# Optimization experiments

Measured on AMD Instinct MI355X. Metric: run time of the kernel, lower is better.

Reference implementation:

```python
import jax, jax.numpy as jnp
import numpy as np

B, T, D = 2, 2048, 1024
H = 16
DK = D // H


def setup_inputs() -> dict:
    key = jax.random.key(0)
    ks = jax.random.split(key, 5)
    s = 1.0 / np.sqrt(D)
    return {
        "x": jax.random.normal(ks[0], (B, T, D), dtype=jnp.float32),
        "Wq": jax.random.normal(ks[1], (D, D), dtype=jnp.float32) * s,
        "bq": jnp.zeros((D,), dtype=jnp.float32),
        "Wk": jax.random.normal(ks[2], (D, D), dtype=jnp.float32) * s,
        "bk": jnp.zeros((D,), dtype=jnp.float32),
        "Wv": jax.random.normal(ks[3], (D, D), dtype=jnp.float32) * s,
        "bv": jnp.zeros((D,), dtype=jnp.float32),
        "Wo": jax.random.normal(ks[4], (D, D), dtype=jnp.float32) * s,
        "bo": jnp.zeros((D,), dtype=jnp.float32),
    }


def reference(x, Wq, bq, Wk, bk, Wv, bv, Wo, bo):
    # projections (torch Linear: x @ W.T + b; here W is stored as (in, out))
    Q = x @ Wq + bq  # (B,T,D)
    K = x @ Wk + bk
    V = x @ Wv + bv
    # split heads -> (B,H,T,dk)
    Q = Q.reshape(B, T, H, DK).transpose(0, 2, 1, 3)
    K = K.reshape(B, T, H, DK).transpose(0, 2, 1, 3)
    V = V.reshape(B, T, H, DK).transpose(0, 2, 1, 3)
    scale = 1.0 / jnp.sqrt(jnp.asarray(DK, dtype=x.dtype))
    scores = jnp.einsum("bhqd,bhkd->bhqk", Q, K) * scale  # (B,H,T,T)
    causal = jnp.tril(jnp.ones((T, T), dtype=bool))
    scores = jnp.where(causal, scores, -jnp.inf)
    weights = jax.nn.softmax(scores, axis=-1)
    # dropout is identity in eval mode
    context = jnp.einsum("bhqk,bhkd->bhqd", weights, V)
    context = context.transpose(0, 2, 1, 3).reshape(B, T, D)
    return context @ Wo + bo
```

## Files before the change

kernel.cpp:

```cpp
#include <hip/hip_runtime.h>
#include <hip/hip_bf16.h>

constexpr int Bc = 2;
constexpr int Tc = 2048;
constexpr int Mc = Bc * Tc;
constexpr float CfQ = 0.18033688011112042f;

typedef __attribute__((ext_vector_type(8))) __bf16 bf16x8;
typedef __attribute__((ext_vector_type(4))) __bf16 bf16x4;
typedef __attribute__((ext_vector_type(4))) float floatx4;

__device__ __forceinline__ void gl_lds16(const void* g, void* l) {
    __builtin_amdgcn_global_load_lds(
        (const __attribute__((address_space(1))) void*)g,
        (__attribute__((address_space(3))) void*)l, 16, 0, 0);
}

__global__ __launch_bounds__(256) void prep_all(const float* __restrict__ x,
                                                const float* __restrict__ Wq,
                                                const float* __restrict__ Wk,
                                                const float* __restrict__ Wv,
                                                const float* __restrict__ Wo,
                                                __bf16* __restrict__ xb,
                                                __bf16* __restrict__ Wqkv,
                                                __bf16* __restrict__ Wot) {
    const int z = blockIdx.z;
    const int tid = threadIdx.x;
    if (z >= 4) {
        const int lb = blockIdx.y * 16 + blockIdx.x;
        const size_t base = ((size_t)(z - 4) * 256 + lb) * 4096;
#pragma unroll
        for (int it = 0; it < 4; ++it) {
            const size_t i = base + (size_t)(it * 256 + tid) * 4;
            const float4 v = *(const float4*)(x + i);
            bf16x4 r;
            r[0] = (__bf16)v.x; r[1] = (__bf16)v.y;
            r[2] = (__bf16)v.z; r[3] = (__bf16)v.w;
            *(bf16x4*)(xb + i) = r;
        }
        return;
    }
    __shared__ float t[64][65];
    const float* W = (z == 0) ? Wq : (z == 1) ? Wk : (z == 2) ? Wv : Wo;
    __bf16* Wt = (z < 3) ? Wqkv + (size_t)z * 1024 * 1024 : Wot;
    const int k0 = blockIdx.y * 64, n0 = blockIdx.x * 64;
    const int c = tid & 63, r0 = tid >> 6;
#pragma unroll
    for (int i = 0; i < 16; ++i)
        t[r0 + i * 4][c] = W[(size_t)(k0 + r0 + i * 4) * 1024 + n0 + c];
    __syncthreads();
#pragma unroll
    for (int i = 0; i < 16; ++i) {
        const int r = r0 + i * 4;
        Wt[(size_t)(n0 + r) * 1024 + k0 + c] = (__bf16)t[c][r];
    }
}

__global__ __launch_bounds__(512, 2) void gemm_qkv(const __bf16* __restrict__ A,
                                                   const __bf16* __restrict__ Bt,
                                                   const float* __restrict__ b0,
                                                   const float* __restrict__ b1,
                                                   const float* __restrict__ b2,
                                                   __bf16* __restrict__ C,
                                                   __bf16* __restrict__ Vt) {
    constexpr int K = 1024, ldc = 2048;
    __shared__ __bf16 As[2][256 * 64];
    __shared__ __bf16 Bs[2][192 * 64];
    const int tid = threadIdx.x, lane = tid & 63, wave = tid >> 6;
    const int wm = wave >> 2, wn = wave & 3;
    const int n = blockIdx.x;
    const int xc = n & 7, ii = n >> 3;
    const int by = 2 * xc + (ii & 1), bx = ii >> 1;
    const int bm = by * 256, bn = bx * 192;
    const __bf16* Ab = A + (size_t)bm * K;
    const __bf16* Bb = Bt + (size_t)bn * K;
    const int quad = lane >> 4, tm = lane & 15;

    floatx4 acc[8][3] = {};

    auto stage = [&](int k0, int sb) {
#pragma unroll
        for (int j = 0; j < 4; ++j) {
            const int s = j * 512 + tid;
            const int row = s >> 3, lc = (s & 7) ^ (row & 7);
            gl_lds16(Ab + (size_t)row * K + k0 + lc * 8, &As[sb][s * 8]);
        }
#pragma unroll
        for (int j = 0; j < 3; ++j) {
            const int s = j * 512 + tid;
            const int row = s >> 3, lc = (s & 7) ^ (row & 7);
            gl_lds16(Bb + (size_t)row * K + k0 + lc * 8, &Bs[sb][s * 8]);
        }
    };

    stage(0, 0);

    for (int st = 0; st < 16; ++st) {
        const int buf = st & 1;
        if (st + 1 < 16) {
            stage((st + 1) * 64, buf ^ 1);
            asm volatile("s_waitcnt vmcnt(7)" ::: "memory");
        } else {
            asm volatile("s_waitcnt vmcnt(0)" ::: "memory");
        }
        __builtin_amdgcn_sched_barrier(0);
        __builtin_amdgcn_s_barrier();

        const __bf16* as = As[buf];
        const __bf16* bs = Bs[buf];
#pragma unroll
        for (int ks = 0; ks < 2; ++ks) {
            bf16x8 bfp[3], afq[8];
#pragma unroll
            for (int n2 = 0; n2 < 3; ++n2) {
                const int r = wn * 48 + n2 * 16 + tm;
                bfp[n2] = *(const bf16x8*)(
                    bs + r * 64 + (((ks * 4 + quad) ^ (r & 7)) * 8));
            }
#pragma unroll
            for (int m8 = 0; m8 < 8; ++m8) {
                const int r = wm * 128 + m8 * 16 + tm;
                afq[m8] = *(const bf16x8*)(
                    as + r * 64 + (((ks * 4 + quad) ^ (r & 7)) * 8));
            }
            __builtin_amdgcn_s_setprio(1);
#pragma unroll
            for (int m8 = 0; m8 < 8; ++m8)
#pragma unroll
                for (int n2 = 0; n2 < 3; ++n2)
                    acc[m8][n2] = __builtin_amdgcn_mfma_f32_16x16x32_bf16(
                        afq[m8], bfp[n2], acc[m8][n2], 0, 0, 0);
            __builtin_amdgcn_s_setprio(0);
        }
        __builtin_amdgcn_sched_barrier(0);
        __builtin_amdgcn_s_barrier();
    }

#pragma unroll
    for (int ni = 0; ni < 3; ++ni) {
        const int gc = bn + wn * 48 + ni * 16 + tm;
        const float bias = (gc < 1024) ? b0[gc]
                         : (gc < 2048) ? b1[gc - 1024]
                                       : b2[gc - 2048];
        const float scale = (gc < 1024) ? CfQ : 1.0f;
#pragma unroll
        for (int mi = 0; mi < 8; ++mi) {
            const int gr0 = bm + wm * 128 + mi * 16 + quad * 4;
            if (gc >= 2048) {
                bf16x4 pv;
#pragma unroll
                for (int r = 0; r < 4; ++r) pv[r] = (__bf16)(acc[mi][ni][r] + bias);
                const int bb = gr0 >> 11, tloc = gr0 & 2047;
                const int hh = (gc - 2048) >> 6, dd = gc & 63;
                const int tperm = (tloc & ~63) + ((tloc >> 2) & 3) * 16 +
                                  ((tloc >> 4) & 3) * 4;
                *(bf16x4*)(Vt + ((size_t)(bb * 16 + hh) * 64 + dd) * 2048 + tperm) = pv;
            } else {
#pragma unroll
                for (int r = 0; r < 4; ++r)
                    C[(size_t)(gr0 + r) * ldc + gc] =
                        (__bf16)((acc[mi][ni][r] + bias) * scale);
            }
        }
    }
}

__global__ __launch_bounds__(256) void gemm_out(const __bf16* __restrict__ A,
                                                const __bf16* __restrict__ Bt,
                                                const float* __restrict__ b0,
                                                float* __restrict__ C) {
    constexpr int TN = 64, NI = 2, K = 1024, ldc = 1024;
    __shared__ __bf16 As[2][128 * 32];
    __shared__ __bf16 Bs[2][TN * 32];
    const int tid = threadIdx.x, lane = tid & 63, wave = tid >> 6;
    const int wm = wave & 1, wn = wave >> 1;
    const int bm = blockIdx.y * 128, bn = blockIdx.x * TN;
    const __bf16* Ab = A + (size_t)bm * K;
    const __bf16* Bb = Bt + (size_t)bn * K;
    const int quad = lane >> 4, tm = lane & 15;
    const int xsw = (tm >> 1) & 3;

    floatx4 acc[4][NI] = {};

    auto stage = [&](int k0, int sbuf) {
#pragma unroll
        for (int i = 0; i < 2; ++i) {
            const int s = i * 256 + tid;
            const int row = s >> 2;
            const int lc = (s & 3) ^ ((row >> 1) & 3);
            gl_lds16(Ab + (size_t)row * K + k0 + lc * 8, &As[sbuf][s * 8]);
        }
        {
            const int s = tid;
            const int row = s >> 2;
            const int lc = (s & 3) ^ ((row >> 1) & 3);
            gl_lds16(Bb + (size_t)row * K + k0 + lc * 8, &Bs[sbuf][s * 8]);
        }
    };

    const int nstep = K >> 5;
    stage(0, 0);
    stage(32, 1);

    for (int ks = 0; ks < nstep; ++ks) {
        const int buf = ks & 1;
        if (ks + 1 < nstep) {
            asm volatile("s_waitcnt vmcnt(3)" ::: "memory");
        } else {
            asm volatile("s_waitcnt vmcnt(0)" ::: "memory");
        }
        __builtin_amdgcn_sched_barrier(0);
        __builtin_amdgcn_s_barrier();

        bf16x8 af[4], bfv[NI];
#pragma unroll
        for (int mi = 0; mi < 4; ++mi)
            af[mi] = *(const bf16x8*)(&As[buf][(wm * 64 + mi * 16 + tm) * 32 +
                                               ((quad ^ xsw) * 8)]);
#pragma unroll
        for (int ni = 0; ni < NI; ++ni)
            bfv[ni] = *(const bf16x8*)(&Bs[buf][(wn * (TN / 2) + ni * 16 + tm) * 32 +
                                                ((quad ^ xsw) * 8)]);
        __builtin_amdgcn_s_setprio(1);
#pragma unroll
        for (int mi = 0; mi < 4; ++mi)
#pragma unroll
            for (int ni = 0; ni < NI; ++ni)
                acc[mi][ni] = __builtin_amdgcn_mfma_f32_16x16x32_bf16(
                    af[mi], bfv[ni], acc[mi][ni], 0, 0, 0);
        __builtin_amdgcn_s_setprio(0);
        __builtin_amdgcn_sched_barrier(0);
        __builtin_amdgcn_s_barrier();
        if (ks + 2 < nstep) stage((ks + 2) * 32, buf);
    }

#pragma unroll
    for (int ni = 0; ni < NI; ++ni) {
        const int gc = bn + wn * (TN / 2) + ni * 16 + tm;
        const float bias = b0[gc];
#pragma unroll
        for (int mi = 0; mi < 4; ++mi) {
            const int gr0 = bm + wm * 64 + mi * 16 + quad * 4;
#pragma unroll
            for (int r = 0; r < 4; ++r)
                C[(size_t)(gr0 + r) * ldc + gc] = acc[mi][ni][r] + bias;
        }
    }
}

__global__ __launch_bounds__(512, 4) void attn_mfma(const __bf16* __restrict__ QK,
                                                    const __bf16* __restrict__ Vt,
                                                    __bf16* __restrict__ ctx) {
    constexpr float NEG = -1e30f;

    __shared__ __bf16 Ks[2][2][64 * 64];
    __shared__ __bf16 Vts[2][2][64 * 64];

    const int tid = threadIdx.x, lane = tid & 63, w = tid >> 6;
    const int g = w >> 2, wq = w & 3;
    const int c = lane & 15, quad = lane >> 4;
    const int n = blockIdx.x;
    const int bh = (n & 7) * 4 + ((n >> 3) & 3);
    const int ip = n >> 5;
    const int b = bh >> 4, h = bh & 15;

    const __bf16* Qb = QK + (size_t)(b * Tc) * 2048 + h * 64;
    const __bf16* Kb = Qb + 1024;
    const __bf16* Vtb = Vt + (size_t)bh * 64 * 2048;

    const int sw = c & 7;
    int koff0[4], koff1[4];
#pragma unroll
    for (int ni = 0; ni < 4; ++ni) {
        const int krow = ni * 16 + c;
        koff0[ni] = krow * 64 + (quad ^ sw) * 8;
        koff1[ni] = krow * 64 + ((4 + quad) ^ sw) * 8;
    }
    int voff[4][2];
#pragma unroll
    for (int di = 0; di < 4; ++di) {
        const int vrow = di * 16 + c;
#pragma unroll
        for (int pr = 0; pr < 2; ++pr)
            voff[di][pr] = vrow * 64 + ((quad * 2 + pr) ^ sw) * 8;
    }

    const int srow = tid >> 3;
    const int slc = (tid & 7) ^ (srow & 7);
    const __bf16* kgB = Kb + (size_t)srow * 2048 + slc * 8;
    const __bf16* vgB = Vtb + (size_t)srow * 2048 + slc * 8;

#pragma unroll 1
    for (int ph = 0; ph < 2; ++ph) {
        const int qt = ph ? 31 - ip : ip;
        const int nk = qt + 1;
        const int npair = (nk + 1) >> 1;

        const __bf16* qr = Qb + (size_t)(qt * 64 + wq * 16 + c) * 2048;
        const bf16x8 qf0 = *(const bf16x8*)(qr + quad * 8);
        const bf16x8 qf1 = *(const bf16x8*)(qr + 32 + quad * 8);

        floatx4 lacc = {};
        floatx4 oa[4] = {};

        auto stage = [&](int p, int sbuf) {
            const __bf16* kg = kgB + (size_t)(2 * p) * 64 * 2048;
            const __bf16* vg = vgB + 2 * p * 64;
            __bf16* kd = &Ks[sbuf][0][tid * 8];
            __bf16* vd = &Vts[sbuf][0][tid * 8];
            gl_lds16(kg, kd);
            gl_lds16(kg + (size_t)64 * 2048, kd + 4096);
            gl_lds16(vg, vd);
            gl_lds16(vg + 64, vd + 4096);
        };

        stage(0, 0);
        if (npair > 1) stage(1, 1);

        for (int kp = 0; kp < npair; ++kp) {
            const int buf = kp & 1;
            if (kp + 1 < npair) {
                asm volatile("s_waitcnt vmcnt(4)" ::: "memory");
            } else {
                asm volatile("s_waitcnt vmcnt(0)" ::: "memory");
            }
            __builtin_amdgcn_sched_barrier(0);
            __builtin_amdgcn_s_barrier();

            const int kt = 2 * kp + g;
            if (kt < nk) {
                const __bf16* ks = Ks[buf][g];
                const __bf16* vs = Vts[buf][g];

                float sv[4][4];
                __builtin_amdgcn_s_setprio(1);
#pragma unroll
                for (int ni = 0; ni < 4; ++ni) {
                    const bf16x8 kb0 = *(const bf16x8*)(ks + koff0[ni]);
                    const bf16x8 kb1 = *(const bf16x8*)(ks + koff1[ni]);
                    floatx4 a = {};
                    a = __builtin_amdgcn_mfma_f32_16x16x32_bf16(kb0, qf0, a, 0, 0, 0);
                    a = __builtin_amdgcn_mfma_f32_16x16x32_bf16(kb1, qf1, a, 0, 0, 0);
#pragma unroll
                    for (int r = 0; r < 4; ++r) sv[ni][r] = a[r];
                }
                __builtin_amdgcn_s_setprio(0);

                if (kt == qt) {
#pragma unroll
                    for (int ni = 0; ni < 4; ++ni)
#pragma unroll
                        for (int r = 0; r < 4; ++r)
                            if (ni * 16 + quad * 4 + r > wq * 16 + c) sv[ni][r] = NEG;
                }
#pragma unroll
                for (int ni = 0; ni < 4; ++ni) {
#pragma unroll
                    for (int r = 0; r < 4; ++r) sv[ni][r] = __builtin_exp2f(sv[ni][r]);
                    lacc[0] += sv[ni][0];
                    lacc[1] += sv[ni][1];
                    lacc[2] += sv[ni][2];
                    lacc[3] += sv[ni][3];
                }

                bf16x8 pb[2];
#pragma unroll
                for (int pr = 0; pr < 2; ++pr)
#pragma unroll
                    for (int j = 0; j < 4; ++j) {
                        pb[pr][j] = (__bf16)sv[pr * 2][j];
                        pb[pr][4 + j] = (__bf16)sv[pr * 2 + 1][j];
                    }

                __builtin_amdgcn_s_setprio(1);
#pragma unroll
                for (int di = 0; di < 4; ++di) {
#pragma unroll
                    for (int pr = 0; pr < 2; ++pr) {
                        const bf16x8 vf = *(const bf16x8*)(vs + voff[di][pr]);
                        oa[di] = __builtin_amdgcn_mfma_f32_16x16x32_bf16(
                            vf, pb[pr], oa[di], 0, 0, 0);
                    }
                }
                __builtin_amdgcn_s_setprio(0);
            }
            __builtin_amdgcn_sched_barrier(0);
            __builtin_amdgcn_s_barrier();
            if (kp + 2 < npair) stage(kp + 2, buf);
        }

        __syncthreads();
        float lsum = lacc[0] + lacc[1] + lacc[2] + lacc[3];
        float* sc = (float*)&Ks[0][0][0];
        if (g == 1) {
#pragma unroll
            for (int di = 0; di < 4; ++di)
                *(floatx4*)(sc + wq * 1088 + di * 256 + lane * 4) = oa[di];
            sc[wq * 1088 + 1024 + lane] = lsum;
        }
        __syncthreads();
        if (g == 0) {
#pragma unroll
            for (int di = 0; di < 4; ++di)
                oa[di] += *(const floatx4*)(sc + wq * 1088 + di * 256 + lane * 4);
            lsum += sc[wq * 1088 + 1024 + lane];
            lsum += __shfl_xor(lsum, 16);
            lsum += __shfl_xor(lsum, 32);
            const float inv = 1.f / lsum;
            __bf16* cp = ctx + (size_t)(b * Tc + qt * 64 + wq * 16 + c) * 1024 +
                         h * 64 + quad * 4;
#pragma unroll
            for (int di = 0; di < 4; ++di) {
                bf16x4 rv;
#pragma unroll
                for (int r = 0; r < 4; ++r) rv[r] = (__bf16)(oa[di][r] * inv);
                *(bf16x4*)(cp + di * 16) = rv;
            }
        }
        __syncthreads();
    }
}

extern "C" void kernel_launch(void* const* d_in, const int* in_sizes, int n_in,
                              void* d_out, int out_size, void* d_ws, size_t ws_size,
                              hipStream_t stream) {
    const float* x  = (const float*)d_in[0];
    const float* Wq = (const float*)d_in[1];
    const float* bq = (const float*)d_in[2];
    const float* Wk = (const float*)d_in[3];
    const float* bk = (const float*)d_in[4];
    const float* Wv = (const float*)d_in[5];
    const float* bv = (const float*)d_in[6];
    const float* Wo = (const float*)d_in[7];
    const float* bo = (const float*)d_in[8];

    __bf16* xb   = (__bf16*)d_ws;
    __bf16* Wqkv = xb + (size_t)Mc * 1024;
    __bf16* Wot  = Wqkv + (size_t)3072 * 1024;
    __bf16* QKb  = Wot + (size_t)1024 * 1024;
    __bf16* Vtw  = QKb + (size_t)Mc * 2048;
    __bf16* ctxb = xb;

    prep_all<<<dim3(16, 16, 8), 256, 0, stream>>>(x, Wq, Wk, Wv, Wo,
                                                  xb, Wqkv, Wot);

    gemm_qkv<<<dim3(256), 512, 0, stream>>>(xb, Wqkv, bq, bk, bv, QKb, Vtw);

    attn_mfma<<<dim3(512), 512, 0, stream>>>(QKb, Vtw, ctxb);

    gemm_out<<<dim3(16, 32), 256, 0, stream>>>(ctxb, Wot, bo, (float*)d_out);
}
```

Before: 179.9 us.

## Switch attention to 32x32x16 MFMA with 4-way key split and new V layout

Rewrites the attention inner loop to use 32x32x16 bf16 MFMA tiles, with each wave covering 32 queries and 32-key tiles. Work is split into four key groups per query pair, and partial results are reduced through LDS in two rounds. The V-transpose layout written by the QKV GEMM changes to match the new fragment order. P fragments are rearranged with lane shuffles. The aim is fewer MFMA instructions and LDS reads per FLOP, at the cost of a longer cross-group reduction and the shuffle overhead.

```diff
diff --git a/kernel.cpp b/kernel.cpp
--- a/kernel.cpp
+++ b/kernel.cpp
@@ -9,11 +9,19 @@
 typedef __attribute__((ext_vector_type(8))) __bf16 bf16x8;
 typedef __attribute__((ext_vector_type(4))) __bf16 bf16x4;
 typedef __attribute__((ext_vector_type(4))) float floatx4;
+typedef __attribute__((ext_vector_type(16))) float f32x16;
+typedef __attribute__((ext_vector_type(4))) unsigned int uint4v;
 
 __device__ __forceinline__ void gl_lds16(const void* g, void* l) {
     __builtin_amdgcn_global_load_lds(
         (const __attribute__((address_space(1))) void*)g,
         (__attribute__((address_space(3))) void*)l, 16, 0, 0);
+}
+
+__device__ __forceinline__ unsigned int pkbf(float x, float y) {
+    union { __bf16 h[2]; unsigned int u; } z;
+    z.h[0] = (__bf16)x; z.h[1] = (__bf16)y;
+    return z.u;
 }
 
 __global__ __launch_bounds__(256) void prep_all(const float* __restrict__ x,
@@ -152,9 +160,10 @@
                 for (int r = 0; r < 4; ++r) pv[r] = (__bf16)(acc[mi][ni][r] + bias);
                 const int bb = gr0 >> 11, tloc = gr0 & 2047;
                 const int hh = (gc - 2048) >> 6, dd = gc & 63;
-                const int tperm = (tloc & ~63) + ((tloc >> 2) & 3) * 16 +
-                                  ((tloc >> 4) & 3) * 4;
-                *(bf16x4*)(Vt + ((size_t)(bb * 16 + hh) * 64 + dd) * 2048 + tperm) = pv;
+                const int tt = tloc >> 5, t5 = tloc & 31;
+                const int u = dd & 31, half = dd >> 5;
+                *(bf16x4*)(Vt + ((size_t)(bb * 16 + hh) * 64 + tt) * 2048 +
+                           u * 64 + half * 32 + t5) = pv;
             } else {
 #pragma unroll
                 for (int r = 0; r < 4; ++r)
@@ -253,12 +262,12 @@
                                                     __bf16* __restrict__ ctx) {
     constexpr float NEG = -1e30f;
 
-    __shared__ __bf16 Ks[2][2][64 * 64];
-    __shared__ __bf16 Vts[2][2][64 * 64];
+    __shared__ __bf16 Ks[2][4][32 * 64];
+    __shared__ __bf16 Vts[2][4][32 * 64];
 
     const int tid = threadIdx.x, lane = tid & 63, w = tid >> 6;
-    const int g = w >> 2, wq = w & 3;
-    const int c = lane & 15, quad = lane >> 4;
+    const int g = w >> 1, ws = w & 1;
+    const int col = lane & 31, hi = lane >> 5;
     const int n = blockIdx.x;
     const int bh = (n & 7) * 4 + ((n >> 3) & 3);
     const int ip = n >> 5;
@@ -266,60 +275,64 @@
 
     const __bf16* Qb = QK + (size_t)(b * Tc) * 2048 + h * 64;
     const __bf16* Kb = Qb + 1024;
-    const __bf16* Vtb = Vt + (size_t)bh * 64 * 2048;
-
-    const int sw = c & 7;
-    int koff0[4], koff1[4];
-#pragma unroll
-    for (int ni = 0; ni < 4; ++ni) {
-        const int krow = ni * 16 + c;
-        koff0[ni] = krow * 64 + (quad ^ sw) * 8;
-        koff1[ni] = krow * 64 + ((4 + quad) ^ sw) * 8;
-    }
-    int voff[4][2];
-#pragma unroll
-    for (int di = 0; di < 4; ++di) {
-        const int vrow = di * 16 + c;
-#pragma unroll
-        for (int pr = 0; pr < 2; ++pr)
-            voff[di][pr] = vrow * 64 + ((quad * 2 + pr) ^ sw) * 8;
-    }
-
-    const int srow = tid >> 3;
-    const int slc = (tid & 7) ^ (srow & 7);
-    const __bf16* kgB = Kb + (size_t)srow * 2048 + slc * 8;
-    const __bf16* vgB = Vtb + (size_t)srow * 2048 + slc * 8;
+    const __bf16* Vtb = Vt + (size_t)bh * 131072;
+
+    const int sw7 = lane & 7;
+    int koff[4], voff[2][2];
+#pragma unroll
+    for (int k16 = 0; k16 < 4; ++k16)
+        koff[k16] = col * 64 + (((k16 * 2 + hi) ^ sw7) * 8);
+#pragma unroll
+    for (int dt = 0; dt < 2; ++dt)
+#pragma unroll
+        for (int tc = 0; tc < 2; ++tc)
+            voff[dt][tc] = col * 64 + (((dt * 4 + tc * 2 + hi) ^ sw7) * 8);
+
+    const __bf16* kK[2];
+    const __bf16* kV[2];
+#pragma unroll
+    for (int j = 0; j < 2; ++j) {
+        const int kc = j * 512 + tid;
+        const int gj = kc >> 8;
+        const int wv = kc & 255;
+        const int r = wv >> 3, lc = (wv & 7) ^ (r & 7);
+        kK[j] = Kb + (size_t)(gj * 32 + r) * 2048 + lc * 8;
+        kV[j] = Vtb + (size_t)gj * 2048 + r * 64 + lc * 8;
+    }
 
 #pragma unroll 1
     for (int ph = 0; ph < 2; ++ph) {
         const int qt = ph ? 31 - ip : ip;
-        const int nk = qt + 1;
-        const int npair = (nk + 1) >> 1;
-
-        const __bf16* qr = Qb + (size_t)(qt * 64 + wq * 16 + c) * 2048;
-        const bf16x8 qf0 = *(const bf16x8*)(qr + quad * 8);
-        const bf16x8 qf1 = *(const bf16x8*)(qr + 32 + quad * 8);
+        const int nkt = 2 * qt + 2;
+        const int niter = (nkt + 3) >> 2;
+        const int ktmax = 2 * qt + ws;
+
+        const __bf16* qr = Qb + (size_t)(qt * 64 + ws * 32 + col) * 2048;
+        bf16x8 qf[4];
+#pragma unroll
+        for (int k16 = 0; k16 < 4; ++k16)
+            qf[k16] = *(const bf16x8*)(qr + k16 * 16 + hi * 8);
 
         floatx4 lacc = {};
-        floatx4 oa[4] = {};
-
-        auto stage = [&](int p, int sbuf) {
-            const __bf16* kg = kgB + (size_t)(2 * p) * 64 * 2048;
-            const __bf16* vg = vgB + 2 * p * 64;
-            __bf16* kd = &Ks[sbuf][0][tid * 8];
-            __bf16* vd = &Vts[sbuf][0][tid * 8];
-            gl_lds16(kg, kd);
-            gl_lds16(kg + (size_t)64 * 2048, kd + 4096);
-            gl_lds16(vg, vd);
-            gl_lds16(vg + 64, vd + 4096);
+        f32x16 oa0 = {}, oa1 = {};
+
+        auto stage = [&](int p, int sb) {
+            __bf16* kd = &Ks[sb][0][0];
+            __bf16* vd = &Vts[sb][0][0];
+#pragma unroll
+            for (int j = 0; j < 2; ++j) {
+                const int kc = j * 512 + tid;
+                gl_lds16(kK[j] + (size_t)p * 128 * 2048, kd + kc * 8);
+                gl_lds16(kV[j] + (size_t)p * 8192, vd + kc * 8);
+            }
         };
 
         stage(0, 0);
-        if (npair > 1) stage(1, 1);
-
-        for (int kp = 0; kp < npair; ++kp) {
+        if (niter > 1) stage(1, 1);
+
+        for (int kp = 0; kp < niter; ++kp) {
             const int buf = kp & 1;
-            if (kp + 1 < npair) {
+            if (kp + 1 < niter) {
                 asm volatile("s_waitcnt vmcnt(4)" ::: "memory");
             } else {
                 asm volatile("s_waitcnt vmcnt(0)" ::: "memory");
@@ -327,95 +340,144 @@
             __builtin_amdgcn_sched_barrier(0);
             __builtin_amdgcn_s_barrier();
 
-            const int kt = 2 * kp + g;
-            if (kt < nk) {
-                const __bf16* ks = Ks[buf][g];
-                const __bf16* vs = Vts[buf][g];
-
-                float sv[4][4];
+            const int kt = 4 * kp + g;
+            if (kt <= ktmax) {
+                const __bf16* ks = &Ks[buf][g][0];
+                const __bf16* vs = &Vts[buf][g][0];
+
+                f32x16 acc = {};
                 __builtin_amdgcn_s_setprio(1);
 #pragma unroll
-                for (int ni = 0; ni < 4; ++ni) {
-                    const bf16x8 kb0 = *(const bf16x8*)(ks + koff0[ni]);
-                    const bf16x8 kb1 = *(const bf16x8*)(ks + koff1[ni]);
-                    floatx4 a = {};
-                    a = __builtin_amdgcn_mfma_f32_16x16x32_bf16(kb0, qf0, a, 0, 0, 0);
-                    a = __builtin_amdgcn_mfma_f32_16x16x32_bf16(kb1, qf1, a, 0, 0, 0);
-#pragma unroll
-                    for (int r = 0; r < 4; ++r) sv[ni][r] = a[r];
+                for (int k16 = 0; k16 < 4; ++k16) {
+                    const bf16x8 kb = *(const bf16x8*)(ks + koff[k16]);
+                    acc = __builtin_amdgcn_mfma_f32_32x32x16_bf16(
+                        kb, qf[k16], acc, 0, 0, 0);
                 }
                 __builtin_amdgcn_s_setprio(0);
 
-                if (kt == qt) {
-#pragma unroll
-                    for (int ni = 0; ni < 4; ++ni)
-#pragma unroll
-                        for (int r = 0; r < 4; ++r)
-                            if (ni * 16 + quad * 4 + r > wq * 16 + c) sv[ni][r] = NEG;
-                }
-#pragma unroll
-                for (int ni = 0; ni < 4; ++ni) {
-#pragma unroll
-                    for (int r = 0; r < 4; ++r) sv[ni][r] = __builtin_exp2f(sv[ni][r]);
-                    lacc[0] += sv[ni][0];
-                    lacc[1] += sv[ni][1];
-                    lacc[2] += sv[ni][2];
-                    lacc[3] += sv[ni][3];
-                }
-
-                bf16x8 pb[2];
-#pragma unroll
-                for (int pr = 0; pr < 2; ++pr)
-#pragma unroll
-                    for (int j = 0; j < 4; ++j) {
-                        pb[pr][j] = (__bf16)sv[pr * 2][j];
-                        pb[pr][4 + j] = (__bf16)sv[pr * 2 + 1][j];
+                if (kt == ktmax) {
+#pragma unroll
+                    for (int reg = 0; reg < 16; ++reg) {
+                        const int crow = (reg & 3) + 8 * (reg >> 2) + 4 * hi;
+                        if (crow > col) acc[reg] = NEG;
                     }
+                }
+#pragma unroll
+                for (int reg = 0; reg < 16; ++reg) {
+                    const float p = __builtin_exp2f(acc[reg]);
+                    acc[reg] = p;
+                    lacc[reg & 3] += p;
+                }
+
+                bf16x8 pf[2];
+#pragma unroll
+                for (int tc = 0; tc < 2; ++tc) {
+                    const int c16 = tc * 8;
+                    const unsigned int a0 = pkbf(acc[c16 + 0], acc[c16 + 1]);
+                    const unsigned int a1 = pkbf(acc[c16 + 2], acc[c16 + 3]);
+                    const unsigned int b0 = pkbf(acc[c16 + 4], acc[c16 + 5]);
+                    const unsigned int b1 = pkbf(acc[c16 + 6], acc[c16 + 7]);
+                    const unsigned int s0 = hi ? a0 : b0, s1 = hi ? a1 : b1;
+                    const unsigned int r0 = __shfl_xor(s0, 32);
+                    const unsigned int r1 = __shfl_xor(s1, 32);
+                    uint4v dv;
+                    dv[0] = hi ? r0 : a0; dv[1] = hi ? r1 : a1;
+                    dv[2] = hi ? b0 : r0; dv[3] = hi ? b1 : r1;
+                    pf[tc] = __builtin_bit_cast(bf16x8, dv);
+                }
 
                 __builtin_amdgcn_s_setprio(1);
 #pragma unroll
-                for (int di = 0; di < 4; ++di) {
-#pragma unroll
-                    for (int pr = 0; pr < 2; ++pr) {
-                        const bf16x8 vf = *(const bf16x8*)(vs + voff[di][pr]);
-                        oa[di] = __builtin_amdgcn_mfma_f32_16x16x32_bf16(
-                            vf, pb[pr], oa[di], 0, 0, 0);
-                    }
+                for (int tc = 0; tc < 2; ++tc) {
+                    const bf16x8 vf0 = *(const bf16x8*)(vs + voff[0][tc]);
+                    oa0 = __builtin_amdgcn_mfma_f32_32x32x16_bf16(
+                        vf0, pf[tc], oa0, 0, 0, 0);
+                    const bf16x8 vf1 = *(const bf16x8*)(vs + voff[1][tc]);
+                    oa1 = __builtin_amdgcn_mfma_f32_32x32x16_bf16(
+                        vf1, pf[tc], oa1, 0, 0, 0);
                 }
                 __builtin_amdgcn_s_setprio(0);
             }
             __builtin_amdgcn_sched_barrier(0);
             __builtin_amdgcn_s_barrier();
-            if (kp + 2 < npair) stage(kp + 2, buf);
+            if (kp + 2 < niter) stage(kp + 2, buf);
         }
 
         __syncthreads();
         float lsum = lacc[0] + lacc[1] + lacc[2] + lacc[3];
-        float* sc = (float*)&Ks[0][0][0];
-        if (g == 1) {
-#pragma unroll
-            for (int di = 0; di < 4; ++di)
-                *(floatx4*)(sc + wq * 1088 + di * 256 + lane * 4) = oa[di];
-            sc[wq * 1088 + 1024 + lane] = lsum;
+        lsum += __shfl_xor(lsum, 32);
+        float* scK = (float*)&Ks[0][0][0];
+        float* scV = (float*)&Vts[0][0][0];
+        const int ob = ws * 2112 + lane * 32;
+        const int lb = ws * 2112 + 2048 + lane;
+        if (g == 1 || g == 3) {
+            float* sc = (g == 1) ? scK : scV;
+#pragma unroll
+            for (int dt = 0; dt < 2; ++dt)
+#pragma unroll
+                for (int a = 0; a < 4; ++a) {
+                    floatx4 t4;
+                    const f32x16& o = dt ? oa1 : oa0;
+                    t4[0] = o[4 * a + 0]; t4[1] = o[4 * a + 1];
+                    t4[2] = o[4 * a + 2]; t4[3] = o[4 * a + 3];
+                    *(floatx4*)(sc + ob + dt * 16 + a * 4) = t4;
+                }
+            sc[lb] = lsum;
+        }
+        __syncthreads();
+        if (g == 0 || g == 2) {
+            const float* sc = (g == 0) ? scK : scV;
+#pragma unroll
+            for (int dt = 0; dt < 2; ++dt)
+#pragma unroll
+                for (int a = 0; a < 4; ++a) {
+                    const floatx4 t4 = *(const floatx4*)(sc + ob + dt * 16 + a * 4);
+                    f32x16& o = dt ? oa1 : oa0;
+                    o[4 * a + 0] += t4[0]; o[4 * a + 1] += t4[1];
+                    o[4 * a + 2] += t4[2]; o[4 * a + 3] += t4[3];
+                }
+            lsum += sc[lb];
+        }
+        __syncthreads();
+        if (g == 2) {
+#pragma unroll
+            for (int dt = 0; dt < 2; ++dt)
+#pragma unroll
+                for (int a = 0; a < 4; ++a) {
+                    floatx4 t4;
+                    const f32x16& o = dt ? oa1 : oa0;
+                    t4[0] = o[4 * a + 0]; t4[1] = o[4 * a + 1];
+                    t4[2] = o[4 * a + 2]; t4[3] = o[4 * a + 3];
+                    *(floatx4*)(scK + ob + dt * 16 + a * 4) = t4;
+                }
+            scK[lb] = lsum;
         }
         __syncthreads();
         if (g == 0) {
 #pragma unroll
-            for (int di = 0; di < 4; ++di)
-                oa[di] += *(const floatx4*)(sc + wq * 1088 + di * 256 + lane * 4);
-            lsum += sc[wq * 1088 + 1024 + lane];
-            lsum += __shfl_xor(lsum, 16);
-            lsum += __shfl_xor(lsum, 32);
+            for (int dt = 0; dt < 2; ++dt)
+#pragma unroll
+                for (int a = 0; a < 4; ++a) {
+                    const floatx4 t4 = *(const floatx4*)(scK + ob + dt * 16 + a * 4);
+                    f32x16& o = dt ? oa1 : oa0;
+                    o[4 * a + 0] += t4[0]; o[4 * a + 1] += t4[1];
+                    o[4 * a + 2] += t4[2]; o[4 * a + 3] += t4[3];
+                }
+            lsum += scK[lb];
             const float inv = 1.f / lsum;
-            __bf16* cp = ctx + (size_t)(b * Tc + qt * 64 + wq * 16 + c) * 1024 +
-                         h * 64 + quad * 4;
-#pragma unroll
-            for (int di = 0; di < 4; ++di) {
-                bf16x4 rv;
-#pragma unroll
-                for (int r = 0; r < 4; ++r) rv[r] = (__bf16)(oa[di][r] * inv);
-                *(bf16x4*)(cp + di * 16) = rv;
-            }
+            __bf16* cp = ctx + (size_t)(b * Tc + qt * 64 + ws * 32 + col) * 1024 +
+                         h * 64 + hi * 4;
+#pragma unroll
+            for (int dt = 0; dt < 2; ++dt)
+#pragma unroll
+                for (int a = 0; a < 4; ++a) {
+                    bf16x4 rv;
+                    const f32x16& o = dt ? oa1 : oa0;
+#pragma unroll
+                    for (int r = 0; r < 4; ++r)
+                        rv[r] = (__bf16)(o[4 * a + r] * inv);
+                    *(bf16x4*)(cp + dt * 32 + a * 8) = rv;
+                }
         }
         __syncthreads();
     }
```

New measurement: 200.4 us. +11.4%, slower.

## Retile output GEMM to 128x128 blocks with BK=64 and swizzled block order

Applied to the files above, without the earlier changes.

The output projection GEMM moves from 128x64 tiles with 256 threads and BK=32 to 128x128 tiles with 512 threads and BK=64. It uses an 8-way XOR LDS swizzle and a grouped block-index remap to improve L2 reuse. The double buffer is now prefetched one step ahead. The aim is higher arithmetic intensity per LDS load and fewer barriers per unit of K. In exchange, the grid drops from 512 blocks to 256 and each block uses more LDS.

```diff
diff --git a/kernel.cpp b/kernel.cpp
--- a/kernel.cpp
+++ b/kernel.cpp
@@ -165,78 +165,85 @@
     }
 }
 
-__global__ __launch_bounds__(256) void gemm_out(const __bf16* __restrict__ A,
-                                                const __bf16* __restrict__ Bt,
-                                                const float* __restrict__ b0,
-                                                float* __restrict__ C) {
-    constexpr int TN = 64, NI = 2, K = 1024, ldc = 1024;
-    __shared__ __bf16 As[2][128 * 32];
-    __shared__ __bf16 Bs[2][TN * 32];
+__global__ __launch_bounds__(512, 2) void gemm_out(const __bf16* __restrict__ A,
+                                                   const __bf16* __restrict__ Bt,
+                                                   const float* __restrict__ b0,
+                                                   float* __restrict__ C) {
+    constexpr int K = 1024, ldc = 1024;
+    __shared__ __bf16 As[2][128 * 64];
+    __shared__ __bf16 Bs[2][128 * 64];
     const int tid = threadIdx.x, lane = tid & 63, wave = tid >> 6;
-    const int wm = wave & 1, wn = wave >> 1;
-    const int bm = blockIdx.y * 128, bn = blockIdx.x * TN;
+    const int wm = wave >> 2, wn = wave & 3;
+    const int n = blockIdx.x;
+    const int by = (n & 7) * 4 + ((n >> 3) & 3), bx = n >> 5;
+    const int bm = by * 128, bn = bx * 128;
     const __bf16* Ab = A + (size_t)bm * K;
     const __bf16* Bb = Bt + (size_t)bn * K;
     const int quad = lane >> 4, tm = lane & 15;
-    const int xsw = (tm >> 1) & 3;
-
-    floatx4 acc[4][NI] = {};
-
-    auto stage = [&](int k0, int sbuf) {
-#pragma unroll
-        for (int i = 0; i < 2; ++i) {
-            const int s = i * 256 + tid;
-            const int row = s >> 2;
-            const int lc = (s & 3) ^ ((row >> 1) & 3);
-            gl_lds16(Ab + (size_t)row * K + k0 + lc * 8, &As[sbuf][s * 8]);
-        }
-        {
-            const int s = tid;
-            const int row = s >> 2;
-            const int lc = (s & 3) ^ ((row >> 1) & 3);
-            gl_lds16(Bb + (size_t)row * K + k0 + lc * 8, &Bs[sbuf][s * 8]);
+
+    floatx4 acc[4][2] = {};
+
+    auto stage = [&](int k0, int sb) {
+#pragma unroll
+        for (int j = 0; j < 2; ++j) {
+            const int s = j * 512 + tid;
+            const int row = s >> 3, lc = (s & 7) ^ (row & 7);
+            gl_lds16(Ab + (size_t)row * K + k0 + lc * 8, &As[sb][s * 8]);
+        }
+#pragma unroll
+        for (int j = 0; j < 2; ++j) {
+            const int s = j * 512 + tid;
+            const int row = s >> 3, lc = (s & 7) ^ (row & 7);
+            gl_lds16(Bb + (size_t)row * K + k0 + lc * 8, &Bs[sb][s * 8]);
         }
     };
 
-    const int nstep = K >> 5;
     stage(0, 0);
-    stage(32, 1);
-
-    for (int ks = 0; ks < nstep; ++ks) {
-        const int buf = ks & 1;
-        if (ks + 1 < nstep) {
-            asm volatile("s_waitcnt vmcnt(3)" ::: "memory");
+
+    for (int st = 0; st < 16; ++st) {
+        const int buf = st & 1;
+        if (st + 1 < 16) {
+            stage((st + 1) * 64, buf ^ 1);
+            asm volatile("s_waitcnt vmcnt(4)" ::: "memory");
         } else {
             asm volatile("s_waitcnt vmcnt(0)" ::: "memory");
         }
         __builtin_amdgcn_sched_barrier(0);
         __builtin_amdgcn_s_barrier();
 
-        bf16x8 af[4], bfv[NI];
-#pragma unroll
-        for (int mi = 0; mi < 4; ++mi)
-            af[mi] = *(const bf16x8*)(&As[buf][(wm * 64 + mi * 16 + tm) * 32 +
-                                               ((quad ^ xsw) * 8)]);
-#pragma unroll
-        for (int ni = 0; ni < NI; ++ni)
-            bfv[ni] = *(const bf16x8*)(&Bs[buf][(wn * (TN / 2) + ni * 16 + tm) * 32 +
-                                                ((quad ^ xsw) * 8)]);
-        __builtin_amdgcn_s_setprio(1);
-#pragma unroll
-        for (int mi = 0; mi < 4; ++mi)
-#pragma unroll
-            for (int ni = 0; ni < NI; ++ni)
-                acc[mi][ni] = __builtin_amdgcn_mfma_f32_16x16x32_bf16(
-                    af[mi], bfv[ni], acc[mi][ni], 0, 0, 0);
-        __builtin_amdgcn_s_setprio(0);
+        const __bf16* as = As[buf];
+        const __bf16* bs = Bs[buf];
+#pragma unroll
+        for (int ks = 0; ks < 2; ++ks) {
+            bf16x8 bfp[2], afq[4];
+#pragma unroll
+            for (int n2 = 0; n2 < 2; ++n2) {
+                const int r = wn * 32 + n2 * 16 + tm;
+                bfp[n2] = *(const bf16x8*)(
+                    bs + r * 64 + (((ks * 4 + quad) ^ (r & 7)) * 8));
+            }
+#pragma unroll
+            for (int m2 = 0; m2 < 4; ++m2) {
+                const int r = wm * 64 + m2 * 16 + tm;
+                afq[m2] = *(const bf16x8*)(
+                    as + r * 64 + (((ks * 4 + quad) ^ (r & 7)) * 8));
+            }
+            __builtin_amdgcn_s_setprio(1);
+#pragma unroll
+            for (int m2 = 0; m2 < 4; ++m2)
+#pragma unroll
+                for (int n2 = 0; n2 < 2; ++n2)
+                    acc[m2][n2] = __builtin_amdgcn_mfma_f32_16x16x32_bf16(
+                        afq[m2], bfp[n2], acc[m2][n2], 0, 0, 0);
+            __builtin_amdgcn_s_setprio(0);
+        }
         __builtin_amdgcn_sched_barrier(0);
         __builtin_amdgcn_s_barrier();
-        if (ks + 2 < nstep) stage((ks + 2) * 32, buf);
-    }
-
-#pragma unroll
-    for (int ni = 0; ni < NI; ++ni) {
-        const int gc = bn + wn * (TN / 2) + ni * 16 + tm;
+    }
+
+#pragma unroll
+    for (int ni = 0; ni < 2; ++ni) {
+        const int gc = bn + wn * 32 + ni * 16 + tm;
         const float bias = b0[gc];
 #pragma unroll
         for (int mi = 0; mi < 4; ++mi) {
@@ -448,5 +455,5 @@
 
     attn_mfma<<<dim3(512), 512, 0, stream>>>(QKb, Vtw, ctxb);
 
-    gemm_out<<<dim3(16, 32), 256, 0, stream>>>(ctxb, Wot, bo, (float*)d_out);
-}
+    gemm_out<<<dim3(256), 512, 0, stream>>>(ctxb, Wot, bo, (float*)d_out);
+}
```

New measurement: 177.5 us, median of 2. Within noise of the previous version (-1.3%).
